# Performance work log

Measured on AMD Instinct MI355X. Metric: run time of the kernel, lower is better.

Reference implementation:

```python
import math
import jax, jax.numpy as jnp
import numpy as np

C_Z = 128
C_HID = 128
B, N = 1, 512


def setup_inputs() -> dict:
    key = jax.random.key(0)
    ks = jax.random.split(key, 8)
    s_in = 1.0 / math.sqrt(C_Z)
    s_hid = 1.0 / math.sqrt(C_HID)
    return {
        "z": jax.random.normal(ks[0], (B, N, N, C_Z), dtype=jnp.float32),
        "residue_mask": jnp.ones((B, N), dtype=jnp.bool_),
        "ln_w": jnp.ones((C_Z,), dtype=jnp.float32),
        "ln_b": jnp.zeros((C_Z,), dtype=jnp.float32),
        "a_w": jax.random.uniform(ks[1], (C_Z, C_HID), jnp.float32, -s_in, s_in),
        "a_b": jax.random.uniform(ks[2], (C_HID,), jnp.float32, -s_in, s_in),
        "b_w": jax.random.uniform(ks[3], (C_Z, C_HID), jnp.float32, -s_in, s_in),
        "b_b": jax.random.uniform(ks[4], (C_HID,), jnp.float32, -s_in, s_in),
        "out_w": jax.random.uniform(ks[5], (C_HID, C_Z), jnp.float32, -s_hid, s_hid),
        "out_b": jax.random.uniform(ks[6], (C_Z,), jnp.float32, -s_hid, s_hid),
    }


def _layernorm(x, w, b, eps=1e-5):
    mu = jnp.mean(x, axis=-1, keepdims=True)
    var = jnp.mean(jnp.square(x - mu), axis=-1, keepdims=True)
    return (x - mu) * jax.lax.rsqrt(var + eps) * w + b


def reference(z, residue_mask, ln_w, ln_b, a_w, a_b, b_w, b_b, out_w, out_b):
    # z: [B, N, N, c_z]
    x = _layernorm(z, ln_w, ln_b)
    a = x @ a_w + a_b  # [B, N, N, c_hid]
    b = x @ b_w + b_b  # [B, N, N, c_hid]
    # outgoing: contract over k -> c_hid independent NxN matmuls
    u = jnp.einsum('bikc,bjkc->bijc', a, b)
    u = (u / math.sqrt(max(z.shape[1], 1))) @ out_w + out_b  # [B, N, N, c_z]
    pair = residue_mask[:, :, None] & residue_mask[:, None, :]  # [B, N, N]
    return u * pair[..., None].astype(u.dtype)
```

## Files before the change

kernel.cpp:

```cpp
#include <hip/hip_runtime.h>

#define NRES 512
#define NN   (NRES * NRES)
#define CZ   128

typedef __attribute__((ext_vector_type(8))) short bf16x8;
typedef __attribute__((ext_vector_type(4))) short s16x4;
typedef __attribute__((ext_vector_type(4))) float f32x4;

static __device__ __forceinline__ short f2bf(float f) {
  union { float f; unsigned u; } v; v.f = f;
  unsigned r = v.u + 0x7fffu + ((v.u >> 16) & 1u);
  return (short)(r >> 16);
}

static __device__ __forceinline__ void gload_lds16(const void* g, void* l) {
  __builtin_amdgcn_global_load_lds(
      (__attribute__((address_space(1))) const void*)g,
      (__attribute__((address_space(3))) void*)l, 16, 0, 0);
}

__global__ __launch_bounds__(256) void k_prep(const float* __restrict__ a_w,
                                              const float* __restrict__ b_w,
                                              const float* __restrict__ out_w,
                                              short* __restrict__ w_cat_t,
                                              short* __restrict__ w_out_t) {
  int idx = blockIdx.x * 256 + threadIdx.x;
  if (idx < 256 * 128) {
    int cc = idx >> 7, zz = idx & 127;
    float v = (cc < 128) ? a_w[zz * 128 + cc] : b_w[zz * 128 + (cc - 128)];
    w_cat_t[idx] = f2bf(v);
  } else if (idx < 256 * 128 + 128 * 128) {
    int i2 = idx - 256 * 128;
    int zz = i2 >> 7, cc = i2 & 127;
    w_out_t[i2] = f2bf(out_w[cc * 128 + zz]);
  }
}

__global__ __launch_bounds__(256) void k_lnproj(const float* __restrict__ z,
                                                const float* __restrict__ ln_w,
                                                const float* __restrict__ ln_b,
                                                const float* __restrict__ a_bias,
                                                const float* __restrict__ b_bias,
                                                const short* __restrict__ w_cat_t,
                                                short* __restrict__ a_t,
                                                short* __restrict__ b_t) {
  __shared__ float xs[64][129];
  __shared__ short xb[64][136];
  __shared__ float part[2][4][64];
  __shared__ float mean_s[64], rstd_s[64];
  __shared__ float lnw_s[128], lnb_s[128];

  const int tid = threadIdx.x;
  const int r0 = blockIdx.x * 64;

  if (tid < 128) { lnw_s[tid] = ln_w[tid]; lnb_s[tid] = ln_b[tid]; }

  const float4* zg = (const float4*)(z + (size_t)r0 * CZ);
#pragma unroll
  for (int it = 0; it < 8; ++it) {
    int idx = tid + it * 256;
    float4 v = zg[idx];
    int row = idx >> 5, c4 = (idx & 31) * 4;
    xs[row][c4] = v.x; xs[row][c4 + 1] = v.y; xs[row][c4 + 2] = v.z; xs[row][c4 + 3] = v.w;
  }
  __syncthreads();

  {
    int row = tid & 63, seg = tid >> 6;
    float s = 0.f, s2 = 0.f;
#pragma unroll
    for (int m = 0; m < 32; ++m) { float v = xs[row][seg * 32 + m]; s += v; s2 += v * v; }
    part[0][seg][row] = s; part[1][seg][row] = s2;
  }
  __syncthreads();
  if (tid < 64) {
    float s  = part[0][0][tid] + part[0][1][tid] + part[0][2][tid] + part[0][3][tid];
    float s2 = part[1][0][tid] + part[1][1][tid] + part[1][2][tid] + part[1][3][tid];
    float mu = s * (1.f / CZ);
    float var = s2 * (1.f / CZ) - mu * mu;
    mean_s[tid] = mu;
    rstd_s[tid] = rsqrtf(var + 1e-5f);
  }
  __syncthreads();
#pragma unroll
  for (int it = 0; it < 32; ++it) {
    int idx = tid + it * 256;
    int row = idx >> 7, k = idx & 127;
    float v = (xs[row][k] - mean_s[row]) * rstd_s[row] * lnw_s[k] + lnb_s[k];
    xb[row][k] = f2bf(v);
  }
  __syncthreads();

  const int w = tid >> 6, l = tid & 63;
  const int q = l >> 4, n16 = l & 15;
  const f32x4 zf = {0.f, 0.f, 0.f, 0.f};
  f32x4 acc[4][4];
#pragma unroll
  for (int a = 0; a < 4; ++a)
#pragma unroll
    for (int b = 0; b < 4; ++b) acc[a][b] = zf;

#pragma unroll
  for (int kk = 0; kk < 4; ++kk) {
    bf16x8 af[4], bfv[4];
#pragma unroll
    for (int rt = 0; rt < 4; ++rt)
      af[rt] = *(const bf16x8*)&xb[rt * 16 + n16][kk * 32 + q * 8];
#pragma unroll
    for (int ct = 0; ct < 4; ++ct) {
      int col = w * 64 + ct * 16 + n16;
      bfv[ct] = *(const bf16x8*)&w_cat_t[col * 128 + kk * 32 + q * 8];
    }
#pragma unroll
    for (int rt = 0; rt < 4; ++rt)
#pragma unroll
      for (int ct = 0; ct < 4; ++ct)
        acc[rt][ct] = __builtin_amdgcn_mfma_f32_16x16x32_bf16(af[rt], bfv[ct], acc[rt][ct], 0, 0, 0);
  }

#pragma unroll
  for (int ct = 0; ct < 4; ++ct) {
    int col = w * 64 + ct * 16 + n16;
    int ch = col & 127;
    short* dst = (col < 128) ? a_t : b_t;
    float bias = (col < 128) ? a_bias[ch] : b_bias[ch];
#pragma unroll
    for (int rt = 0; rt < 4; ++rt) {
      s16x4 pk;
#pragma unroll
      for (int rg = 0; rg < 4; ++rg) pk[rg] = f2bf(acc[rt][ct][rg] + bias);
      *(s16x4*)&dst[(size_t)ch * NN + r0 + rt * 16 + q * 4] = pk;
    }
  }
}

__global__ __launch_bounds__(256) void k_einsum(const short* __restrict__ a_t,
                                                const short* __restrict__ b_t,
                                                short* __restrict__ u_bf) {
  __shared__ short As[128 * 32], Bs[128 * 32];

  const int bid = blockIdx.x;
  const int xcd = bid & 7;
  const int g = bid >> 3;
  const int c = (xcd << 4) | (g >> 4);
  const int t = g & 15;
  const int ti = t >> 2, tj = t & 3;

  const short* Ab = a_t + (size_t)c * NN + (size_t)(ti * 128) * NRES;
  const short* Bb = b_t + (size_t)c * NN + (size_t)(tj * 128) * NRES;

  const int tid = threadIdx.x, w = tid >> 6, l = tid & 63;
  const int q = l >> 4, n16 = l & 15;
  const int wr = w >> 1, wc = w & 1;

  const int srow0 = w * 32 + (l >> 2);
  const int slot = l & 3;

  const f32x4 zf = {0.f, 0.f, 0.f, 0.f};
  f32x4 acc[4][4];
#pragma unroll
  for (int a = 0; a < 4; ++a)
#pragma unroll
    for (int b = 0; b < 4; ++b) acc[a][b] = zf;

  for (int kk = 0; kk < 16; ++kk) {
    const int k0 = kk * 32;
    __syncthreads();
    {
      int r1 = srow0, r2 = srow0 + 16;
      int g1 = slot ^ ((r1 >> 1) & 3);
      int g2 = slot ^ ((r2 >> 1) & 3);
      gload_lds16(Ab + (size_t)r1 * NRES + k0 + g1 * 8, &As[r1 * 32 + slot * 8]);
      gload_lds16(Ab + (size_t)r2 * NRES + k0 + g2 * 8, &As[r2 * 32 + slot * 8]);
      gload_lds16(Bb + (size_t)r1 * NRES + k0 + g1 * 8, &Bs[r1 * 32 + slot * 8]);
      gload_lds16(Bb + (size_t)r2 * NRES + k0 + g2 * 8, &Bs[r2 * 32 + slot * 8]);
    }
    __syncthreads();

    bf16x8 af[4], bfv[4];
#pragma unroll
    for (int rt = 0; rt < 4; ++rt) {
      int m = wr * 64 + rt * 16 + n16;
      af[rt] = *(const bf16x8*)&As[m * 32 + (q ^ ((m >> 1) & 3)) * 8];
    }
#pragma unroll
    for (int ct = 0; ct < 4; ++ct) {
      int n = wc * 64 + ct * 16 + n16;
      bfv[ct] = *(const bf16x8*)&Bs[n * 32 + (q ^ ((n >> 1) & 3)) * 8];
    }
#pragma unroll
    for (int rt = 0; rt < 4; ++rt)
#pragma unroll
      for (int ct = 0; ct < 4; ++ct)
        acc[rt][ct] = __builtin_amdgcn_mfma_f32_16x16x32_bf16(af[rt], bfv[ct], acc[rt][ct], 0, 0, 0);
  }

  short* ub = u_bf + (size_t)c * NN + (size_t)(ti * 128) * NRES + tj * 128;
  const float s = 0.04419417382415922f;
#pragma unroll
  for (int rt = 0; rt < 4; ++rt)
#pragma unroll
    for (int ct = 0; ct < 4; ++ct) {
      int il = wr * 64 + rt * 16 + q * 4;
      int jl = wc * 64 + ct * 16 + n16;
#pragma unroll
      for (int rg = 0; rg < 4; ++rg)
        ub[(size_t)(il + rg) * NRES + jl] = f2bf(acc[rt][ct][rg] * s);
    }
}

__global__ __launch_bounds__(256) void k_outproj(const short* __restrict__ u_bf,
                                                 const short* __restrict__ w_out_t,
                                                 const float* __restrict__ out_b,
                                                 const int* __restrict__ mask,
                                                 float* __restrict__ out) {
  __shared__ short Ut[128 * 136];

  const int m0 = blockIdx.x * 128;
  const int tid = threadIdx.x, w = tid >> 6, l = tid & 63;
  const int q = l >> 4, n16 = l & 15;
  const int wr = w >> 1, wc = w & 1;

  {
    const int c0 = (tid & 63) * 2;
    const int mg = w * 32;
    const short* g0 = u_bf + (size_t)c0 * NN + m0 + mg;
    const short* g1 = g0 + NN;
#pragma unroll
    for (int v = 0; v < 4; ++v) {
      bf16x8 x0 = *(const bf16x8*)(g0 + v * 8);
      bf16x8 x1 = *(const bf16x8*)(g1 + v * 8);
#pragma unroll
      for (int j = 0; j < 8; ++j) {
        int m = mg + v * 8 + j;
        int pk = ((int)(unsigned short)x1[j] << 16) | (unsigned short)x0[j];
        *(int*)&Ut[m * 136 + c0] = pk;
      }
    }
  }
  __syncthreads();

  const f32x4 zf = {0.f, 0.f, 0.f, 0.f};
  f32x4 acc[4][4];
#pragma unroll
  for (int a = 0; a < 4; ++a)
#pragma unroll
    for (int b = 0; b < 4; ++b) acc[a][b] = zf;

#pragma unroll
  for (int kk = 0; kk < 4; ++kk) {
    bf16x8 af[4], bfv[4];
#pragma unroll
    for (int rt = 0; rt < 4; ++rt) {
      int m = wr * 64 + rt * 16 + n16;
      af[rt] = *(const bf16x8*)&Ut[m * 136 + kk * 32 + q * 8];
    }
#pragma unroll
    for (int ct = 0; ct < 4; ++ct) {
      int zc = wc * 64 + ct * 16 + n16;
      bfv[ct] = *(const bf16x8*)&w_out_t[zc * 128 + kk * 32 + q * 8];
    }
#pragma unroll
    for (int rt = 0; rt < 4; ++rt)
#pragma unroll
      for (int ct = 0; ct < 4; ++ct)
        acc[rt][ct] = __builtin_amdgcn_mfma_f32_16x16x32_bf16(af[rt], bfv[ct], acc[rt][ct], 0, 0, 0);
  }

  const int i_blk = m0 >> 9;
  const int j0 = m0 & 511;
  const int mi = mask[i_blk];
#pragma unroll
  for (int ct = 0; ct < 4; ++ct) {
    int zc = wc * 64 + ct * 16 + n16;
    float bias = out_b[zc];
#pragma unroll
    for (int rt = 0; rt < 4; ++rt) {
      int mloc = wr * 64 + rt * 16 + q * 4;
#pragma unroll
      for (int rg = 0; rg < 4; ++rg) {
        int m = m0 + mloc + rg;
        int jj = j0 + mloc + rg;
        float val = acc[rt][ct][rg] + bias;
        if (!(mi != 0 && mask[jj] != 0)) val = 0.f;
        out[(size_t)m * CZ + zc] = val;
      }
    }
  }
}

extern "C" void kernel_launch(void* const* d_in, const int* in_sizes, int n_in,
                              void* d_out, int out_size, void* d_ws, size_t ws_size,
                              hipStream_t stream) {
  const float* z     = (const float*)d_in[0];
  const int*   mask  = (const int*)d_in[1];
  const float* ln_w  = (const float*)d_in[2];
  const float* ln_b  = (const float*)d_in[3];
  const float* a_w   = (const float*)d_in[4];
  const float* a_b   = (const float*)d_in[5];
  const float* b_w   = (const float*)d_in[6];
  const float* b_b   = (const float*)d_in[7];
  const float* out_w = (const float*)d_in[8];
  const float* out_b = (const float*)d_in[9];
  float* out = (float*)d_out;

  char* p = (char*)d_ws;
  short* w_cat_t = (short*)p; p += (size_t)256 * 128 * 2;
  short* w_out_t = (short*)p; p += (size_t)128 * 128 * 2;
  short* a_t  = (short*)p; p += (size_t)NN * 128 * 2;
  short* b_t  = (short*)p; p += (size_t)NN * 128 * 2;
  short* u_bf = (short*)p; p += (size_t)NN * 128 * 2;

  hipLaunchKernelGGL(k_prep,    dim3(192),  dim3(256), 0, stream, a_w, b_w, out_w, w_cat_t, w_out_t);
  hipLaunchKernelGGL(k_lnproj,  dim3(4096), dim3(256), 0, stream, z, ln_w, ln_b, a_b, b_b, w_cat_t, a_t, b_t);
  hipLaunchKernelGGL(k_einsum,  dim3(2048), dim3(256), 0, stream, a_t, b_t, u_bf);
  hipLaunchKernelGGL(k_outproj, dim3(2048), dim3(256), 0, stream, u_bf, w_out_t, out_b, mask, out);
}
```

Before: 425.6 us.

## Rework LN in registers, deepen einsum K-tile, transpose outproj for vector stores

k_lnproj now keeps each row's z values in registers and reduces mean and variance with lane shuffles, removing the fp32 LDS staging buffer and several barriers. k_einsum loads a 64-wide K slab per barrier pair, with an XOR swizzle over 8 chunks, which halves the number of sync rounds. k_outproj swaps the MFMA operands so each lane writes float4 rows of the output instead of scalar strided stores, at the cost of gathering 8 scalar LDS reads per B fragment. All three kernels add an occupancy hint of 3 blocks in launch_bounds.

Measured after the change: 382.7 us. -10.1%, faster.

```diff
diff --git a/kernel.cpp b/kernel.cpp
--- a/kernel.cpp
+++ b/kernel.cpp
@@ -37,58 +37,47 @@
   }
 }
 
-__global__ __launch_bounds__(256) void k_lnproj(const float* __restrict__ z,
-                                                const float* __restrict__ ln_w,
-                                                const float* __restrict__ ln_b,
-                                                const float* __restrict__ a_bias,
-                                                const float* __restrict__ b_bias,
-                                                const short* __restrict__ w_cat_t,
-                                                short* __restrict__ a_t,
-                                                short* __restrict__ b_t) {
-  __shared__ float xs[64][129];
+__global__ __launch_bounds__(256, 3) void k_lnproj(const float* __restrict__ z,
+                                                   const float* __restrict__ ln_w,
+                                                   const float* __restrict__ ln_b,
+                                                   const float* __restrict__ a_bias,
+                                                   const float* __restrict__ b_bias,
+                                                   const short* __restrict__ w_cat_t,
+                                                   short* __restrict__ a_t,
+                                                   short* __restrict__ b_t) {
   __shared__ short xb[64][136];
-  __shared__ float part[2][4][64];
-  __shared__ float mean_s[64], rstd_s[64];
-  __shared__ float lnw_s[128], lnb_s[128];
 
   const int tid = threadIdx.x;
   const int r0 = blockIdx.x * 64;
-
-  if (tid < 128) { lnw_s[tid] = ln_w[tid]; lnb_s[tid] = ln_b[tid]; }
+  const int row = tid >> 2, seg = tid & 3;
 
   const float4* zg = (const float4*)(z + (size_t)r0 * CZ);
+  float4 v[8];
+#pragma unroll
+  for (int it = 0; it < 8; ++it) v[it] = zg[row * 32 + seg + it * 4];
+
+  float s = 0.f, s2 = 0.f;
 #pragma unroll
   for (int it = 0; it < 8; ++it) {
-    int idx = tid + it * 256;
-    float4 v = zg[idx];
-    int row = idx >> 5, c4 = (idx & 31) * 4;
-    xs[row][c4] = v.x; xs[row][c4 + 1] = v.y; xs[row][c4 + 2] = v.z; xs[row][c4 + 3] = v.w;
-  }
-  __syncthreads();
-
-  {
-    int row = tid & 63, seg = tid >> 6;
-    float s = 0.f, s2 = 0.f;
-#pragma unroll
-    for (int m = 0; m < 32; ++m) { float v = xs[row][seg * 32 + m]; s += v; s2 += v * v; }
-    part[0][seg][row] = s; part[1][seg][row] = s2;
-  }
-  __syncthreads();
-  if (tid < 64) {
-    float s  = part[0][0][tid] + part[0][1][tid] + part[0][2][tid] + part[0][3][tid];
-    float s2 = part[1][0][tid] + part[1][1][tid] + part[1][2][tid] + part[1][3][tid];
-    float mu = s * (1.f / CZ);
-    float var = s2 * (1.f / CZ) - mu * mu;
-    mean_s[tid] = mu;
-    rstd_s[tid] = rsqrtf(var + 1e-5f);
-  }
-  __syncthreads();
-#pragma unroll
-  for (int it = 0; it < 32; ++it) {
-    int idx = tid + it * 256;
-    int row = idx >> 7, k = idx & 127;
-    float v = (xs[row][k] - mean_s[row]) * rstd_s[row] * lnw_s[k] + lnb_s[k];
-    xb[row][k] = f2bf(v);
+    s  += v[it].x + v[it].y + v[it].z + v[it].w;
+    s2 += v[it].x * v[it].x + v[it].y * v[it].y + v[it].z * v[it].z + v[it].w * v[it].w;
+  }
+  s  += __shfl_xor(s, 1);  s  += __shfl_xor(s, 2);
+  s2 += __shfl_xor(s2, 1); s2 += __shfl_xor(s2, 2);
+  const float mu = s * (1.f / CZ);
+  const float rstd = rsqrtf(s2 * (1.f / CZ) - mu * mu + 1e-5f);
+
+  const float4* lw4 = (const float4*)ln_w;
+  const float4* lb4 = (const float4*)ln_b;
+#pragma unroll
+  for (int it = 0; it < 8; ++it) {
+    float4 wv = lw4[seg + it * 4], bv = lb4[seg + it * 4];
+    s16x4 pk;
+    pk[0] = f2bf((v[it].x - mu) * rstd * wv.x + bv.x);
+    pk[1] = f2bf((v[it].y - mu) * rstd * wv.y + bv.y);
+    pk[2] = f2bf((v[it].z - mu) * rstd * wv.z + bv.z);
+    pk[3] = f2bf((v[it].w - mu) * rstd * wv.w + bv.w);
+    *(s16x4*)&xb[row][seg * 4 + it * 16] = pk;
   }
   __syncthreads();
 
@@ -135,10 +124,10 @@
   }
 }
 
-__global__ __launch_bounds__(256) void k_einsum(const short* __restrict__ a_t,
-                                                const short* __restrict__ b_t,
-                                                short* __restrict__ u_bf) {
-  __shared__ short As[128 * 32], Bs[128 * 32];
+__global__ __launch_bounds__(256, 3) void k_einsum(const short* __restrict__ a_t,
+                                                   const short* __restrict__ b_t,
+                                                   short* __restrict__ u_bf) {
+  __shared__ short As[128 * 64], Bs[128 * 64];
 
   const int bid = blockIdx.x;
   const int xcd = bid & 7;
@@ -154,8 +143,9 @@
   const int q = l >> 4, n16 = l & 15;
   const int wr = w >> 1, wc = w & 1;
 
-  const int srow0 = w * 32 + (l >> 2);
-  const int slot = l & 3;
+  const int srow = l >> 3;
+  const int schk = l & 7;
+  const int gchk = schk ^ srow;
 
   const f32x4 zf = {0.f, 0.f, 0.f, 0.f};
   f32x4 acc[4][4];
@@ -164,36 +154,36 @@
 #pragma unroll
     for (int b = 0; b < 4; ++b) acc[a][b] = zf;
 
-  for (int kk = 0; kk < 16; ++kk) {
-    const int k0 = kk * 32;
+  for (int st = 0; st < 8; ++st) {
+    const int k0 = st * 64;
     __syncthreads();
-    {
-      int r1 = srow0, r2 = srow0 + 16;
-      int g1 = slot ^ ((r1 >> 1) & 3);
-      int g2 = slot ^ ((r2 >> 1) & 3);
-      gload_lds16(Ab + (size_t)r1 * NRES + k0 + g1 * 8, &As[r1 * 32 + slot * 8]);
-      gload_lds16(Ab + (size_t)r2 * NRES + k0 + g2 * 8, &As[r2 * 32 + slot * 8]);
-      gload_lds16(Bb + (size_t)r1 * NRES + k0 + g1 * 8, &Bs[r1 * 32 + slot * 8]);
-      gload_lds16(Bb + (size_t)r2 * NRES + k0 + g2 * 8, &Bs[r2 * 32 + slot * 8]);
+#pragma unroll
+    for (int i = 0; i < 4; ++i) {
+      int r = w * 32 + i * 8 + srow;
+      gload_lds16(Ab + (size_t)r * NRES + k0 + gchk * 8, &As[(w * 32 + i * 8) * 64 + l * 8]);
+      gload_lds16(Bb + (size_t)r * NRES + k0 + gchk * 8, &Bs[(w * 32 + i * 8) * 64 + l * 8]);
     }
     __syncthreads();
 
-    bf16x8 af[4], bfv[4];
-#pragma unroll
-    for (int rt = 0; rt < 4; ++rt) {
-      int m = wr * 64 + rt * 16 + n16;
-      af[rt] = *(const bf16x8*)&As[m * 32 + (q ^ ((m >> 1) & 3)) * 8];
-    }
-#pragma unroll
-    for (int ct = 0; ct < 4; ++ct) {
-      int n = wc * 64 + ct * 16 + n16;
-      bfv[ct] = *(const bf16x8*)&Bs[n * 32 + (q ^ ((n >> 1) & 3)) * 8];
-    }
-#pragma unroll
-    for (int rt = 0; rt < 4; ++rt)
-#pragma unroll
-      for (int ct = 0; ct < 4; ++ct)
-        acc[rt][ct] = __builtin_amdgcn_mfma_f32_16x16x32_bf16(af[rt], bfv[ct], acc[rt][ct], 0, 0, 0);
+#pragma unroll
+    for (int kk = 0; kk < 2; ++kk) {
+      bf16x8 af[4], bfv[4];
+#pragma unroll
+      for (int rt = 0; rt < 4; ++rt) {
+        int m = wr * 64 + rt * 16 + n16;
+        af[rt] = *(const bf16x8*)&As[m * 64 + ((kk * 4 + q) ^ (m & 7)) * 8];
+      }
+#pragma unroll
+      for (int ct = 0; ct < 4; ++ct) {
+        int n = wc * 64 + ct * 16 + n16;
+        bfv[ct] = *(const bf16x8*)&Bs[n * 64 + ((kk * 4 + q) ^ (n & 7)) * 8];
+      }
+#pragma unroll
+      for (int rt = 0; rt < 4; ++rt)
+#pragma unroll
+        for (int ct = 0; ct < 4; ++ct)
+          acc[rt][ct] = __builtin_amdgcn_mfma_f32_16x16x32_bf16(af[rt], bfv[ct], acc[rt][ct], 0, 0, 0);
+    }
   }
 
   short* ub = u_bf + (size_t)c * NN + (size_t)(ti * 128) * NRES + tj * 128;
@@ -210,32 +200,31 @@
     }
 }
 
-__global__ __launch_bounds__(256) void k_outproj(const short* __restrict__ u_bf,
-                                                 const short* __restrict__ w_out_t,
-                                                 const float* __restrict__ out_b,
-                                                 const int* __restrict__ mask,
-                                                 float* __restrict__ out) {
-  __shared__ short Ut[128 * 136];
+#define US_S 130
+__global__ __launch_bounds__(256, 3) void k_outproj(const short* __restrict__ u_bf,
+                                                    const short* __restrict__ w_out_t,
+                                                    const float* __restrict__ out_b,
+                                                    const int* __restrict__ mask,
+                                                    float* __restrict__ out) {
+  __shared__ short Us[128 * US_S];
 
   const int m0 = blockIdx.x * 128;
   const int tid = threadIdx.x, w = tid >> 6, l = tid & 63;
   const int q = l >> 4, n16 = l & 15;
-  const int wr = w >> 1, wc = w & 1;
+  const int wz = w >> 1, wm = w & 1;
 
   {
-    const int c0 = (tid & 63) * 2;
-    const int mg = w * 32;
-    const short* g0 = u_bf + (size_t)c0 * NN + m0 + mg;
-    const short* g1 = g0 + NN;
-#pragma unroll
-    for (int v = 0; v < 4; ++v) {
-      bf16x8 x0 = *(const bf16x8*)(g0 + v * 8);
-      bf16x8 x1 = *(const bf16x8*)(g1 + v * 8);
-#pragma unroll
-      for (int j = 0; j < 8; ++j) {
-        int m = mg + v * 8 + j;
-        int pk = ((int)(unsigned short)x1[j] << 16) | (unsigned short)x0[j];
-        *(int*)&Ut[m * 136 + c0] = pk;
+    const int mseg = tid & 15;
+    const int cb = tid >> 4;
+#pragma unroll
+    for (int it = 0; it < 8; ++it) {
+      int cc = it * 16 + cb;
+      bf16x8 vv = *(const bf16x8*)(u_bf + (size_t)cc * NN + m0 + mseg * 8);
+      int base = cc * US_S + mseg * 8;
+#pragma unroll
+      for (int wi = 0; wi < 4; ++wi) {
+        int pk = ((int)(unsigned short)vv[2 * wi + 1] << 16) | (unsigned short)vv[2 * wi];
+        *(int*)&Us[base + 2 * wi] = pk;
       }
     }
   }
@@ -250,16 +239,21 @@
 
 #pragma unroll
   for (int kk = 0; kk < 4; ++kk) {
-    bf16x8 af[4], bfv[4];
+    bf16x8 af[4];
 #pragma unroll
     for (int rt = 0; rt < 4; ++rt) {
-      int m = wr * 64 + rt * 16 + n16;
-      af[rt] = *(const bf16x8*)&Ut[m * 136 + kk * 32 + q * 8];
-    }
+      int zz = wz * 64 + rt * 16 + n16;
+      af[rt] = *(const bf16x8*)&w_out_t[zz * 128 + kk * 32 + q * 8];
+    }
+    bf16x8 bfv[4];
 #pragma unroll
     for (int ct = 0; ct < 4; ++ct) {
-      int zc = wc * 64 + ct * 16 + n16;
-      bfv[ct] = *(const bf16x8*)&w_out_t[zc * 128 + kk * 32 + q * 8];
+      int mm = wm * 64 + ct * 16 + n16;
+      int c0 = kk * 32 + q * 8;
+      bf16x8 tv;
+#pragma unroll
+      for (int j = 0; j < 8; ++j) tv[j] = Us[(c0 + j) * US_S + mm];
+      bfv[ct] = tv;
     }
 #pragma unroll
     for (int rt = 0; rt < 4; ++rt)
@@ -273,19 +267,18 @@
   const int mi = mask[i_blk];
 #pragma unroll
   for (int ct = 0; ct < 4; ++ct) {
-    int zc = wc * 64 + ct * 16 + n16;
-    float bias = out_b[zc];
+    int mm = wm * 64 + ct * 16 + n16;
+    int on = (mi != 0) && (mask[j0 + mm] != 0);
 #pragma unroll
     for (int rt = 0; rt < 4; ++rt) {
-      int mloc = wr * 64 + rt * 16 + q * 4;
-#pragma unroll
-      for (int rg = 0; rg < 4; ++rg) {
-        int m = m0 + mloc + rg;
-        int jj = j0 + mloc + rg;
-        float val = acc[rt][ct][rg] + bias;
-        if (!(mi != 0 && mask[jj] != 0)) val = 0.f;
-        out[(size_t)m * CZ + zc] = val;
-      }
+      int z0 = wz * 64 + rt * 16 + q * 4;
+      float4 bias = *(const float4*)&out_b[z0];
+      float4 r;
+      r.x = on ? acc[rt][ct][0] + bias.x : 0.f;
+      r.y = on ? acc[rt][ct][1] + bias.y : 0.f;
+      r.z = on ? acc[rt][ct][2] + bias.z : 0.f;
+      r.w = on ? acc[rt][ct][3] + bias.w : 0.f;
+      *(float4*)&out[(size_t)(m0 + mm) * CZ + z0] = r;
     }
   }
 }
```
